# Performance work log

Measured on AMD Instinct MI355X. Metric: run time of the kernel, lower is better.

Reference implementation:

```python
import jax, jax.numpy as jnp
import numpy as np

WS, SS, P, H = 7, 3, 14, 12  # window, shift, patch grid, heads
NW = (P // WS) ** 2          # windows per image = 4
N_WIN = WS * WS              # tokens per window = 49

def _rel_pos_index():
    coords = np.stack(np.meshgrid(np.arange(WS), np.arange(WS), indexing='ij')).reshape(2, -1)
    rel = (coords[:, :, None] - coords[:, None, :]).transpose(1, 2, 0).astype(np.int64)
    rel[..., 0] += WS - 1
    rel[..., 1] += WS - 1
    rel[..., 0] *= 2 * WS - 1
    return rel.sum(-1)  # [49,49]

def _shift_mask():
    img = np.zeros((P, P))
    sl = (slice(0, -WS), slice(-WS, -SS), slice(-SS, None))
    cnt = 0
    for h in sl:
        for w in sl:
            img[h, w] = cnt
            cnt += 1
    mw = img.reshape(P // WS, WS, P // WS, WS).transpose(0, 2, 1, 3).reshape(-1, N_WIN)
    am = mw[:, None, :] - mw[:, :, None]
    return np.where(am != 0, -100.0, 0.0).astype(np.float32)  # [nW,49,49]

RPI = jnp.asarray(_rel_pos_index())
MASK = jnp.asarray(_shift_mask())

def _hswish(x):
    return x * jnp.clip(x + 3.0, 0.0, 6.0) / 6.0

def _hsig(x):
    return jnp.clip(x + 3.0, 0.0, 6.0) / 6.0

def _bn(x, g, b, eps=1e-5):
    # training-mode batchnorm over (B,H,W) per channel, biased variance
    m = x.mean((0, 2, 3), keepdims=True)
    v = ((x - m) ** 2).mean((0, 2, 3), keepdims=True)
    return (x - m) / jnp.sqrt(v + eps) * g[None, :, None, None] + b[None, :, None, None]

def setup_inputs() -> dict:
    key = jax.random.key(0)
    ks = jax.random.split(key, 20)
    C, HID = 768, 3072
    return {
        'x': jax.random.normal(ks[0], (32, 197, C), jnp.float32),
        'w_qkv': jax.random.normal(ks[1], (3 * C, C), jnp.float32) * 0.02,
        'w_proj': jax.random.normal(ks[2], (C, C), jnp.float32) * 0.02,
        'b_proj': jax.random.normal(ks[3], (C,), jnp.float32) * 0.02,
        'rpb_table': jax.random.normal(ks[4], ((2 * WS - 1) ** 2, H), jnp.float32) * 0.02,
        'pw1_w': jax.random.normal(ks[5], (HID, C), jnp.float32) * 0.02,
        'bn1_g': 1.0 + jax.random.normal(ks[6], (HID,), jnp.float32) * 0.02,
        'bn1_b': jax.random.normal(ks[7], (HID,), jnp.float32) * 0.02,
        'dw_w': jax.random.normal(ks[8], (HID, 3, 3), jnp.float32) * 0.1,
        'bn2_g': 1.0 + jax.random.normal(ks[9], (HID,), jnp.float32) * 0.02,
        'bn2_b': jax.random.normal(ks[10], (HID,), jnp.float32) * 0.02,
        'se_w1': jax.random.normal(ks[11], (HID // 4, HID), jnp.float32) * 0.02,
        'se_b1': jax.random.normal(ks[12], (HID // 4,), jnp.float32) * 0.02,
        'se_w2': jax.random.normal(ks[13], (HID, HID // 4), jnp.float32) * 0.02,
        'se_b2': jax.random.normal(ks[14], (HID,), jnp.float32) * 0.02,
        'pw2_w': jax.random.normal(ks[15], (C, HID), jnp.float32) * 0.02,
        'bn3_g': 1.0 + jax.random.normal(ks[16], (C,), jnp.float32) * 0.02,
        'bn3_b': jax.random.normal(ks[17], (C,), jnp.float32) * 0.02,
    }

def reference(x, w_qkv, w_proj, b_proj, rpb_table, pw1_w, bn1_g, bn1_b, dw_w,
              bn2_g, bn2_b, se_w1, se_b1, se_w2, se_b2, pw2_w, bn3_g, bn3_b):
    B, N, C = x.shape
    hd = C // H
    scale = hd ** -0.5
    nw = P // WS

    cls_tok = x[:, :1]
    xs = x[:, 1:].reshape(B, P, P, C)
    xs = jnp.roll(xs, (-SS, -SS), axis=(1, 2))  # cyclic shift
    # window partition -> [B*nW, 49, C]
    win = xs.reshape(B, nw, WS, nw, WS, C).transpose(0, 1, 3, 2, 4, 5).reshape(B * NW, N_WIN, C)

    qkv = (win @ w_qkv.T).reshape(B * NW, N_WIN, 3, H, hd).transpose(2, 0, 3, 1, 4)
    q, k, v = qkv[0], qkv[1], qkv[2]  # [B*nW, H, 49, hd]
    attn = jnp.einsum('bhqd,bhkd->bhqk', q, k) * scale
    # relative position bias gather: [H,49,49]
    bias = rpb_table[RPI.reshape(-1)].reshape(N_WIN, N_WIN, H).transpose(2, 0, 1)
    attn = attn + bias[None]
    # shifted-window mask add
    attn = (attn.reshape(B, NW, H, N_WIN, N_WIN) + MASK[None, :, None]).reshape(B * NW, H, N_WIN, N_WIN)
    attn = jax.nn.softmax(attn, axis=-1)
    out = jnp.einsum('bhqk,bhkd->bhqd', attn, v).transpose(0, 2, 1, 3).reshape(B * NW, N_WIN, C)
    out = out @ w_proj.T + b_proj

    # window reverse + reverse shift
    xs = out.reshape(B, nw, nw, WS, WS, C).transpose(0, 1, 3, 2, 4, 5).reshape(B, P, P, C)
    xs = jnp.roll(xs, (SS, SS), axis=(1, 2))
    x = jnp.concatenate([cls_tok, xs.reshape(B, P * P, C)], axis=1)

    # LocalityFeedForward (inverted residual conv MLP with SE)
    cls_tok, xt = x[:, :1], x[:, 1:]
    f = xt.transpose(0, 2, 1).reshape(B, C, P, P)
    h = _hswish(_bn(jnp.einsum('bchw,oc->bohw', f, pw1_w), bn1_g, bn1_b))
    h = _hswish(_bn(jax.lax.conv_general_dilated(
        h, dw_w[:, None], (1, 1), 'SAME',
        feature_group_count=h.shape[1],
        dimension_numbers=('NCHW', 'OIHW', 'NCHW')), bn2_g, bn2_b))
    s = h.mean((2, 3))  # global avg pool [B, hid]
    s = _hsig(jax.nn.relu(s @ se_w1.T + se_b1) @ se_w2.T + se_b2)
    h = h * s[:, :, None, None]
    h = _bn(jnp.einsum('bchw,oc->bohw', h, pw2_w), bn3_g, bn3_b)
    f = f + h
    x = jnp.concatenate([cls_tok, f.reshape(B, C, P * P).transpose(0, 2, 1)], axis=1)
    return x
```

## Files before the change

kernel.cpp:

```cpp
#include <hip/hip_runtime.h>
#include <hip/hip_bf16.h>

typedef unsigned short ushort_t;
typedef unsigned int uint_t;
typedef short short8 __attribute__((ext_vector_type(8)));
typedef float floatx4 __attribute__((ext_vector_type(4)));

__device__ inline float b2f(ushort_t u){
    uint_t v = ((uint_t)u) << 16;
    return __uint_as_float(v);
}
__device__ inline ushort_t f2b(float f){
    uint_t v = __float_as_uint(f);
    uint_t r = (v + 0x7FFFu + ((v >> 16) & 1u)) >> 16;
    return (ushort_t)r;
}
__device__ inline void unpack8(uint4 u, float* f){
    uint_t w[4] = {u.x, u.y, u.z, u.w};
    #pragma unroll
    for (int i = 0; i < 4; ++i){
        f[2*i]   = __uint_as_float(w[i] << 16);
        f[2*i+1] = __uint_as_float(w[i] & 0xFFFF0000u);
    }
}
__device__ inline uint4 pack8(const float* f){
    uint4 o;
    uint_t w[4];
    #pragma unroll
    for (int i = 0; i < 4; ++i)
        w[i] = (uint_t)f2b(f[2*i]) | ((uint_t)f2b(f[2*i+1]) << 16);
    o.x = w[0]; o.y = w[1]; o.z = w[2]; o.w = w[3];
    return o;
}
__device__ inline ushort4 cvt4(float4 v){
    ushort4 o;
    o.x = f2b(v.x); o.y = f2b(v.y); o.z = f2b(v.z); o.w = f2b(v.w);
    return o;
}
__device__ inline float hswish(float y){
    return y * fminf(fmaxf(y + 3.f, 0.f), 6.f) * (1.f/6.f);
}

#define MROWS 6272
#define CDIM  768
#define HID   3072
#define QKV3  2304

__device__ inline int scatter_row(int ri){
    int w  = ri / 49, t = ri % 49;
    int b  = w >> 2,  wi = w & 3;
    int wy = wi >> 1, wx = wi & 1;
    int ty = t / 7,   tx = t % 7;
    int yd = (wy*7 + ty + 3) % 14;
    int xd = (wx*7 + tx + 3) % 14;
    return b*196 + yd*14 + xd;
}

__global__ __launch_bounds__(256) void cvt_f2b(const float4* __restrict__ in,
                                               ushort4* __restrict__ out, int n4){
    int i = blockIdx.x * 256 + threadIdx.x;
    if (i < n4) out[i] = cvt4(in[i]);
}

__global__ __launch_bounds__(256) void dw_transpose(const float* __restrict__ w,
                                                    float* __restrict__ wT){
    int i = blockIdx.x*256 + threadIdx.x;
    if (i < HID*9){ int c = i/9, k = i%9; wT[k*HID + c] = w[i]; }
}

__global__ __launch_bounds__(256) void gather_win(const float4* __restrict__ x,
                                                  ushort4* __restrict__ win){
    int idx = blockIdx.x * 256 + threadIdx.x;
    if (idx >= MROWS * 192) return;
    int r  = idx / 192, c4 = idx % 192;
    int w  = r / 49,  t  = r % 49;
    int b  = w >> 2,  wi = w & 3;
    int wy = wi >> 1, wx = wi & 1;
    int ty = t / 7,   tx = t % 7;
    int ys = (wy*7 + ty + 3) % 14;
    int xs = (wx*7 + tx + 3) % 14;
    win[idx] = cvt4(x[(size_t)b*197*192 + (size_t)(1 + ys*14 + xs)*192 + c4]);
}

__global__ __launch_bounds__(256) void gemm_bt(const ushort_t* __restrict__ A,
                                               const ushort_t* __restrict__ B,
                                               ushort_t* __restrict__ Cb,
                                               float* __restrict__ Cf,
                                               int M, int N, int K,
                                               const float* __restrict__ bias,
                                               float* __restrict__ stats,
                                               int scat){
    const int nx   = gridDim.x;
    int flat = blockIdx.y * nx + blockIdx.x;
    int xcd  = flat & 7;
    int k    = flat >> 3;
    int by   = xcd + 8 * (k / nx);
    int bx   = k % nx;
    if (by * 128 >= M) return;

    __shared__ __align__(16) ushort_t As[2][128*32];
    __shared__ __align__(16) ushort_t Bs[2][128*32];
    const int tid  = threadIdx.x;
    const int lane = tid & 63;
    const int wid  = tid >> 6;
    const int m0 = by * 128;
    const int n0 = bx * 128;
    const int wm = (wid >> 1) * 64;
    const int wn = (wid & 1) * 64;

    const int srow = (lane >> 2);
    const int scol = (((lane & 3) ^ ((lane >> 3) & 3)) * 8);

    floatx4 acc[4][4] = {};

    auto stage = [&](int buf, int k0){
        #pragma unroll
        for (int j = 0; j < 2; ++j){
            int ch  = wid*2 + j;
            const ushort_t* gA = A + (size_t)(m0 + ch*16 + srow)*K + k0 + scol;
            const ushort_t* gB = B + (size_t)(n0 + ch*16 + srow)*K + k0 + scol;
            __builtin_amdgcn_global_load_lds(
                (const __attribute__((address_space(1))) void*)gA,
                (__attribute__((address_space(3))) void*)(&As[buf][ch*512 + lane*8]), 16, 0, 0);
            __builtin_amdgcn_global_load_lds(
                (const __attribute__((address_space(1))) void*)gB,
                (__attribute__((address_space(3))) void*)(&Bs[buf][ch*512 + lane*8]), 16, 0, 0);
        }
    };

    const int NK = K >> 5;
    stage(0, 0);

    const int fr   = lane & 15;
    const int quad = lane >> 4;
    const int cosw = (quad ^ ((fr >> 1) & 3)) * 8;
    int cur = 0;
    for (int it = 0; it < NK; ++it){
        __builtin_amdgcn_sched_barrier(0);
        __builtin_amdgcn_s_barrier();
        if (it + 1 < NK){
            stage(cur ^ 1, (it + 1) << 5);
            asm volatile("s_waitcnt vmcnt(4)" ::: "memory");
        } else {
            asm volatile("s_waitcnt vmcnt(0)" ::: "memory");
        }
        __builtin_amdgcn_s_barrier();
        __builtin_amdgcn_sched_barrier(0);

        short8 af[4], bfr[4];
        #pragma unroll
        for (int i = 0; i < 4; ++i){
            af[i]  = *(const short8*)(&As[cur][(wm + i*16 + fr)*32 + cosw]);
            bfr[i] = *(const short8*)(&Bs[cur][(wn + i*16 + fr)*32 + cosw]);
        }
        #pragma unroll
        for (int i = 0; i < 4; ++i)
            #pragma unroll
            for (int j = 0; j < 4; ++j)
                acc[i][j] = __builtin_amdgcn_mfma_f32_16x16x32_bf16(af[i], bfr[j], acc[i][j], 0, 0, 0);
        cur ^= 1;
    }

    if (!scat && Cb){
        __syncthreads();
        ushort_t* Cspace = (wid < 2) ? &As[0][0] : &Bs[0][0];
        #pragma unroll
        for (int i = 0; i < 4; ++i){
            #pragma unroll
            for (int j = 0; j < 4; ++j){
                int col = wn + j*16 + fr;
                float bv = bias ? bias[n0 + col] : 0.f;
                #pragma unroll
                for (int r = 0; r < 4; ++r)
                    Cspace[(i*16 + quad*4 + r)*128 + (col ^ (quad << 4))] =
                        f2b(acc[i][j][r] + bv);
            }
        }
        __syncthreads();
        #pragma unroll
        for (int q = 0; q < 8; ++q){
            int fl  = q*256 + tid;
            int row = fl >> 4, u4c = fl & 15;
            const ushort_t* srcRow = (row < 64) ? (&As[0][0] + row*128)
                                                : (&Bs[0][0] + (row - 64)*128);
            int g = (row >> 2) & 3;
            *(uint4*)(Cb + (size_t)(m0 + row)*N + n0 + u4c*8) =
                *(const uint4*)(srcRow + ((u4c*8) ^ (g << 4)));
        }
    } else {
        #pragma unroll
        for (int i = 0; i < 4; ++i){
            int grow = m0 + wm + i*16 + quad*4;
            #pragma unroll
            for (int j = 0; j < 4; ++j){
                int gcol = n0 + wn + j*16 + fr;
                float bv = bias ? bias[gcol] : 0.f;
                if (scat){
                    #pragma unroll
                    for (int r = 0; r < 4; ++r){
                        float v = acc[i][j][r] + bv;
                        size_t off = (size_t)scatter_row(grow + r)*N + gcol;
                        Cf[off] = v;
                        Cb[off] = f2b(v);
                    }
                } else {
                    #pragma unroll
                    for (int r = 0; r < 4; ++r)
                        Cf[(size_t)(grow + r)*N + gcol] = acc[i][j][r] + bv;
                }
            }
        }
    }

    if (stats){
        #pragma unroll
        for (int j = 0; j < 4; ++j){
            int gcol = n0 + wn + j*16 + fr;
            float bv = bias ? bias[gcol] : 0.f;
            float sv = 0.f, sq = 0.f;
            #pragma unroll
            for (int i = 0; i < 4; ++i)
                #pragma unroll
                for (int r = 0; r < 4; ++r){
                    float v = acc[i][j][r] + bv;
                    sv += v; sq += v*v;
                }
            sv += __shfl_xor(sv, 16, 64);  sq += __shfl_xor(sq, 16, 64);
            sv += __shfl_xor(sv, 32, 64);  sq += __shfl_xor(sq, 32, 64);
            if (lane < 16){
                atomicAdd(&stats[gcol], sv);
                atomicAdd(&stats[N + gcol], sq);
            }
        }
    }
}

__global__ __launch_bounds__(256) void gemm_bt64(const ushort_t* __restrict__ A,
                                                 const ushort_t* __restrict__ B,
                                                 ushort_t* __restrict__ Cb,
                                                 float* __restrict__ Cf,
                                                 int M, int N, int K,
                                                 const float* __restrict__ bias,
                                                 float* __restrict__ stats,
                                                 int scat){
    const int nx   = gridDim.x;
    int flat = blockIdx.y * nx + blockIdx.x;
    int xcd  = flat & 7;
    int k    = flat >> 3;
    int by   = xcd + 8 * (k / nx);
    int bx   = k % nx;
    if (by * 128 >= M) return;

    __shared__ __align__(16) ushort_t As[2][128*32];
    __shared__ __align__(16) ushort_t Bs[2][64*32];
    const int tid  = threadIdx.x;
    const int lane = tid & 63;
    const int wid  = tid >> 6;
    const int m0 = by * 128;
    const int n0 = bx * 64;
    const int wm = (wid >> 1) * 64;
    const int wn = (wid & 1) * 32;

    const int srow = (lane >> 2);
    const int scol = (((lane & 3) ^ ((lane >> 3) & 3)) * 8);

    floatx4 acc[4][2] = {};

    auto stage = [&](int buf, int k0){
        #pragma unroll
        for (int j = 0; j < 2; ++j){
            int ch = wid*2 + j;
            const ushort_t* gA = A + (size_t)(m0 + ch*16 + srow)*K + k0 + scol;
            __builtin_amdgcn_global_load_lds(
                (const __attribute__((address_space(1))) void*)gA,
                (__attribute__((address_space(3))) void*)(&As[buf][ch*512 + lane*8]), 16, 0, 0);
        }
        const ushort_t* gB = B + (size_t)(n0 + wid*16 + srow)*K + k0 + scol;
        __builtin_amdgcn_global_load_lds(
            (const __attribute__((address_space(1))) void*)gB,
            (__attribute__((address_space(3))) void*)(&Bs[buf][wid*512 + lane*8]), 16, 0, 0);
    };

    const int NK = K >> 5;
    stage(0, 0);

    const int fr   = lane & 15;
    const int quad = lane >> 4;
    const int cosw = (quad ^ ((fr >> 1) & 3)) * 8;
    int cur = 0;
    for (int it = 0; it < NK; ++it){
        __builtin_amdgcn_sched_barrier(0);
        __builtin_amdgcn_s_barrier();
        if (it + 1 < NK){
            stage(cur ^ 1, (it + 1) << 5);
            asm volatile("s_waitcnt vmcnt(3)" ::: "memory");
        } else {
            asm volatile("s_waitcnt vmcnt(0)" ::: "memory");
        }
        __builtin_amdgcn_s_barrier();
        __builtin_amdgcn_sched_barrier(0);

        short8 af[4], bfr[2];
        #pragma unroll
        for (int i = 0; i < 4; ++i)
            af[i]  = *(const short8*)(&As[cur][(wm + i*16 + fr)*32 + cosw]);
        #pragma unroll
        for (int j = 0; j < 2; ++j)
            bfr[j] = *(const short8*)(&Bs[cur][(wn + j*16 + fr)*32 + cosw]);
        #pragma unroll
        for (int i = 0; i < 4; ++i)
            #pragma unroll
            for (int j = 0; j < 2; ++j)
                acc[i][j] = __builtin_amdgcn_mfma_f32_16x16x32_bf16(af[i], bfr[j], acc[i][j], 0, 0, 0);
        cur ^= 1;
    }

    #pragma unroll
    for (int i = 0; i < 4; ++i){
        int grow = m0 + wm + i*16 + quad*4;
        #pragma unroll
        for (int j = 0; j < 2; ++j){
            int gcol = n0 + wn + j*16 + fr;
            float bv = bias ? bias[gcol] : 0.f;
            if (scat){
                #pragma unroll
                for (int r = 0; r < 4; ++r){
                    float v = acc[i][j][r] + bv;
                    size_t off = (size_t)scatter_row(grow + r)*N + gcol;
                    Cf[off] = v;
                    Cb[off] = f2b(v);
                }
            } else if (Cb){
                #pragma unroll
                for (int r = 0; r < 4; ++r)
                    Cb[(size_t)(grow + r)*N + gcol] = f2b(acc[i][j][r] + bv);
            } else {
                #pragma unroll
                for (int r = 0; r < 4; ++r)
                    Cf[(size_t)(grow + r)*N + gcol] = acc[i][j][r] + bv;
            }
        }
    }

    if (stats){
        #pragma unroll
        for (int j = 0; j < 2; ++j){
            int gcol = n0 + wn + j*16 + fr;
            float bv = bias ? bias[gcol] : 0.f;
            float sv = 0.f, sq = 0.f;
            #pragma unroll
            for (int i = 0; i < 4; ++i)
                #pragma unroll
                for (int r = 0; r < 4; ++r){
                    float v = acc[i][j][r] + bv;
                    sv += v; sq += v*v;
                }
            sv += __shfl_xor(sv, 16, 64);  sq += __shfl_xor(sq, 16, 64);
            sv += __shfl_xor(sv, 32, 64);  sq += __shfl_xor(sq, 32, 64);
            if (lane < 16){
                atomicAdd(&stats[gcol], sv);
                atomicAdd(&stats[N + gcol], sq);
            }
        }
    }
}

__global__ __launch_bounds__(256) void bm_precompute(const float* __restrict__ rpb,
                                                     float* __restrict__ bm){
    int idx = blockIdx.x*256 + threadIdx.x;
    if (idx >= 12*4*64*64) return;
    int ki = idx & 63, qi = (idx >> 6) & 63, wi = (idx >> 12) & 3, h = idx >> 14;
    float v = -1e30f;
    if (qi < 49 && ki < 49){
        int qy = qi/7, qx = qi%7, ky = ki/7, kx = ki%7;
        int ridx = (qy - ky + 6)*13 + (qx - kx + 6);
        v = rpb[ridx*12 + h];
        int wy = wi >> 1, wx = wi & 1;
        int gqy = wy*7 + qy, gqx = wx*7 + qx, gky = wy*7 + ky, gkx = wx*7 + kx;
        int cq = ((gqy < 7) ? 0 : (gqy < 11 ? 1 : 2))*3 + ((gqx < 7) ? 0 : (gqx < 11 ? 1 : 2));
        int ck = ((gky < 7) ? 0 : (gky < 11 ? 1 : 2))*3 + ((gkx < 7) ? 0 : (gkx < 11 ? 1 : 2));
        if (cq != ck) v -= 100.f;
    }
    bm[idx] = v;
}

__global__ __launch_bounds__(256) void attn_mfma(const ushort_t* __restrict__ qkv,
                                                 ushort_t* __restrict__ outp,
                                                 const float* __restrict__ bm){
    __shared__ __align__(16) ushort_t Ps[64*72];
    __shared__ __align__(16) ushort_t VT[64*72];
    const int tid = threadIdx.x, lane = tid & 63, wid = tid >> 6;
    const int h = blockIdx.x, w = blockIdx.y, wi = w & 3;
    const int fr = lane & 15, quad = lane >> 4, co = quad*8;

    for (int idx = tid; idx < 64*8; idx += 256){
        int k = idx >> 3, ng = idx & 7;
        uint4 u = {0u, 0u, 0u, 0u};
        if (k < 49) u = *(const uint4*)(qkv + (size_t)(w*49 + k)*QKV3 + 1536 + h*64 + ng*8);
        const ushort_t* vp = (const ushort_t*)&u;
        #pragma unroll
        for (int e = 0; e < 8; ++e) VT[(ng*8 + e)*72 + k] = vp[e];
    }
    __syncthreads();

    floatx4 accs[4] = {};
    const ushort_t* qbase = qkv + (size_t)(w*49 + wid*16 + fr)*QKV3 + h*64;
    #pragma unroll
    for (int k0 = 0; k0 < 64; k0 += 32){
        short8 af = *(const short8*)(qbase + k0 + co);
        #pragma unroll
        for (int j = 0; j < 4; ++j){
            const ushort_t* kbase = qkv + (size_t)(w*49 + j*16 + fr)*QKV3 + 768 + h*64;
            short8 bf = *(const short8*)(kbase + k0 + co);
            accs[j] = __builtin_amdgcn_mfma_f32_16x16x32_bf16(af, bf, accs[j], 0, 0, 0);
        }
    }

    const float* bmh = bm + (size_t)((h*4 + wi)*64 + wid*16)*64;
    #pragma unroll
    for (int r = 0; r < 4; ++r){
        int lrow = quad*4 + r;
        float m = -3e38f;
        #pragma unroll
        for (int j = 0; j < 4; ++j){
            float a = accs[j][r]*0.125f + bmh[lrow*64 + j*16 + fr];
            accs[j][r] = a;
            m = fmaxf(m, a);
        }
        #pragma unroll
        for (int off = 1; off < 16; off <<= 1) m = fmaxf(m, __shfl_xor(m, off, 64));
        float s = 0.f;
        #pragma unroll
        for (int j = 0; j < 4; ++j){
            float e = __expf(accs[j][r] - m);
            accs[j][r] = e; s += e;
        }
        #pragma unroll
        for (int off = 1; off < 16; off <<= 1) s += __shfl_xor(s, off, 64);
        float inv = 1.f / s;
        #pragma unroll
        for (int j = 0; j < 4; ++j)
            Ps[(wid*16 + lrow)*72 + j*16 + fr] = f2b(accs[j][r]*inv);
    }
    __syncthreads();

    floatx4 acco[4] = {};
    #pragma unroll
    for (int k0 = 0; k0 < 64; k0 += 32){
        short8 af = *(const short8*)(Ps + (wid*16 + fr)*72 + k0 + co);
        #pragma unroll
        for (int j = 0; j < 4; ++j){
            short8 bf = *(const short8*)(VT + (j*16 + fr)*72 + k0 + co);
            acco[j] = __builtin_amdgcn_mfma_f32_16x16x32_bf16(af, bf, acco[j], 0, 0, 0);
        }
    }
    #pragma unroll
    for (int r = 0; r < 4; ++r){
        int qi = wid*16 + quad*4 + r;
        if (qi < 49){
            #pragma unroll
            for (int j = 0; j < 4; ++j)
                outp[(size_t)(w*49 + qi)*CDIM + h*64 + j*16 + fr] = f2b(acco[j][r]);
        }
    }
}

__global__ void zero_f32(float* __restrict__ p, int n){
    int i = blockIdx.x*256 + threadIdx.x;
    if (i < n) p[i] = 0.f;
}
__global__ __launch_bounds__(256) void bn_stats_v(const ushort_t* __restrict__ X,
                                                  float* __restrict__ sums){
    const int cgl = threadIdx.x & 31;
    const int rp  = threadIdx.x >> 5;
    const int cg  = blockIdx.x*32 + cgl;
    const int r0  = blockIdx.y*224;
    const uint4* Xb = (const uint4*)X;
    float s[8] = {}, q[8] = {};
    for (int r = r0 + rp; r < r0 + 224; r += 8){
        uint4 u = Xb[(size_t)r*384 + cg];
        float f[8]; unpack8(u, f);
        #pragma unroll
        for (int e = 0; e < 8; ++e){ s[e] += f[e]; q[e] += f[e]*f[e]; }
    }
    #pragma unroll
    for (int e = 0; e < 8; ++e){
        s[e] += __shfl_xor(s[e], 32, 64);
        q[e] += __shfl_xor(q[e], 32, 64);
    }
    __shared__ float red[4][32][17];
    const int wv = threadIdx.x >> 6;
    if ((threadIdx.x & 32) == 0){
        #pragma unroll
        for (int e = 0; e < 8; ++e){
            red[wv][cgl][e]   = s[e];
            red[wv][cgl][8+e] = q[e];
        }
    }
    __syncthreads();
    #pragma unroll
    for (int k = 0; k < 2; ++k){
        int o = threadIdx.x*2 + k;
        int cgo = o >> 4, e = o & 15;
        float v = red[0][cgo][e] + red[1][cgo][e] + red[2][cgo][e] + red[3][cgo][e];
        int c = blockIdx.x*256 + cgo*8 + (e & 7);
        atomicAdd(&sums[(e < 8 ? 0 : HID) + c], v);
    }
}
__global__ void bn_finalize(float* __restrict__ sums, const float* __restrict__ g,
                            const float* __restrict__ b, int Cch){
    int c = blockIdx.x*256 + threadIdx.x;
    if (c >= Cch) return;
    float mean = sums[c] * (1.f/6272.f);
    float var  = sums[Cch + c] * (1.f/6272.f) - mean*mean;
    float sc = g[c] * rsqrtf(var + 1e-5f);
    sums[c] = sc;
    sums[Cch + c] = b[c] - mean*sc;
}

__global__ __launch_bounds__(256) void dwconv_v(const ushort_t* __restrict__ in,
                                                const float* __restrict__ wT,
                                                const float* __restrict__ ss,
                                                ushort_t* __restrict__ out){
    int idx = blockIdx.x*256 + threadIdx.x;
    if (idx >= MROWS*384) return;
    int r  = idx / 384, cg = idx % 384;
    int b  = r / 196,  p  = r % 196;
    int y  = p / 14,   x  = p % 14;
    int c  = cg*8;
    const uint4* inb = (const uint4*)(in + (size_t)b*196*HID);
    float sc[8], sh[8];
    {
        const float4* s0 = (const float4*)(ss + c);
        const float4* s1 = (const float4*)(ss + HID + c);
        float4 a0 = s0[0], a1 = s0[1], b0 = s1[0], b1 = s1[1];
        sc[0]=a0.x; sc[1]=a0.y; sc[2]=a0.z; sc[3]=a0.w;
        sc[4]=a1.x; sc[5]=a1.y; sc[6]=a1.z; sc[7]=a1.w;
        sh[0]=b0.x; sh[1]=b0.y; sh[2]=b0.z; sh[3]=b0.w;
        sh[4]=b1.x; sh[5]=b1.y; sh[6]=b1.z; sh[7]=b1.w;
    }
    float acc[8] = {};
    #pragma unroll
    for (int ky = 0; ky < 3; ++ky){
        int yy = y + ky - 1;
        if ((unsigned)yy >= 14u) continue;
        #pragma unroll
        for (int kx = 0; kx < 3; ++kx){
            int xx = x + kx - 1;
            if ((unsigned)xx >= 14u) continue;
            uint4 u = inb[(yy*14 + xx)*384 + cg];
            float fin[8]; unpack8(u, fin);
            const float4* wp = (const float4*)(wT + (ky*3 + kx)*HID + c);
            float4 w0 = wp[0], w1 = wp[1];
            float wv[8] = {w0.x,w0.y,w0.z,w0.w,w1.x,w1.y,w1.z,w1.w};
            #pragma unroll
            for (int e = 0; e < 8; ++e)
                acc[e] += hswish(fin[e]*sc[e] + sh[e]) * wv[e];
        }
    }
    ((uint4*)out)[idx] = pack8(acc);
}

__global__ __launch_bounds__(256) void se_mean_v(const ushort_t* __restrict__ X,
                                                 const float* __restrict__ ss,
                                                 float* __restrict__ s){
    const int b   = blockIdx.x;
    const int cgl = threadIdx.x & 31;
    const int rp  = threadIdx.x >> 5;
    const int cg  = blockIdx.y*32 + cgl;
    const int c   = cg*8;
    float sc[8], sh[8];
    #pragma unroll
    for (int e = 0; e < 8; ++e){ sc[e] = ss[c+e]; sh[e] = ss[HID+c+e]; }
    const uint4* Xb = (const uint4*)(X + (size_t)b*196*HID);
    float a[8] = {};
    for (int p = rp; p < 196; p += 8){
        uint4 u = Xb[(size_t)p*384 + cg];
        float f[8]; unpack8(u, f);
        #pragma unroll
        for (int e = 0; e < 8; ++e) a[e] += hswish(f[e]*sc[e] + sh[e]);
    }
    #pragma unroll
    for (int e = 0; e < 8; ++e) a[e] += __shfl_xor(a[e], 32, 64);
    __shared__ float red[4][32][9];
    const int wv = threadIdx.x >> 6;
    if ((threadIdx.x & 32) == 0){
        #pragma unroll
        for (int e = 0; e < 8; ++e) red[wv][cgl][e] = a[e];
    }
    __syncthreads();
    {
        int o = threadIdx.x;
        int cgo = o >> 3, e = o & 7;
        float v = red[0][cgo][e] + red[1][cgo][e] + red[2][cgo][e] + red[3][cgo][e];
        s[(size_t)b*HID + blockIdx.y*256 + cgo*8 + e] = v * (1.f/196.f);
    }
}
__global__ __launch_bounds__(256) void se_fc(const float* __restrict__ in,
                                             const float* __restrict__ w,
                                             const float* __restrict__ bias,
                                             float* __restrict__ out,
                                             int IN, int OUT, int mode){
    int wv   = (blockIdx.x*256 + threadIdx.x) >> 6;
    int lane = threadIdx.x & 63;
    if (wv >= OUT) return;
    const float* wr = w + (size_t)wv * IN;
    float acc[32];
    #pragma unroll
    for (int b = 0; b < 32; ++b) acc[b] = 0.f;
    for (int k = lane; k < IN; k += 64){
        float wval = wr[k];
        #pragma unroll
        for (int b = 0; b < 32; ++b)
            acc[b] += in[b*IN + k] * wval;
    }
    #pragma unroll
    for (int b = 0; b < 32; ++b){
        float v = acc[b];
        #pragma unroll
        for (int off = 32; off; off >>= 1) v += __shfl_down(v, off, 64);
        if (lane == 0){
            float a = v + bias[wv];
            if (mode == 0) a = fmaxf(a, 0.f);
            else           a = fminf(fmaxf(a + 3.f, 0.f), 6.f) * (1.f/6.f);
            out[b*OUT + wv] = a;
        }
    }
}
__global__ __launch_bounds__(256) void se_scale(ushort_t* __restrict__ X,
                                                const float* __restrict__ ss,
                                                const float* __restrict__ s2){
    int idx = blockIdx.x*256 + threadIdx.x;
    if (idx >= MROWS * (HID/8)) return;
    int r = idx / (HID/8), c8 = idx % (HID/8);
    int b = r / 196;
    int c = c8*8;
    uint4 u = ((uint4*)X)[idx];
    float f[8]; unpack8(u, f);
    const float* sp = s2 + b*HID + c;
    #pragma unroll
    for (int e = 0; e < 8; ++e)
        f[e] = hswish(f[e]*ss[c+e] + ss[HID+c+e]) * sp[e];
    ((uint4*)X)[idx] = pack8(f);
}

__global__ __launch_bounds__(256) void final_k(const float4* __restrict__ xin,
                                               const float4* __restrict__ f,
                                               const float4* __restrict__ h4,
                                               const float* __restrict__ ss,
                                               float4* __restrict__ outp){
    int idx = blockIdx.x*256 + threadIdx.x;
    if (idx >= 32*197*192) return;
    int b = idx / (197*192);
    int rem = idx % (197*192);
    int n = rem / 192, c4 = rem % 192;
    if (n == 0){ outp[idx] = xin[idx]; return; }
    size_t off = ((size_t)b*196 + n - 1)*192 + c4;
    float4 hv = h4[off];
    float4 fv = f[off];
    float4 o;
    int c = c4*4;
    o.x = fv.x + hv.x*ss[c+0] + ss[CDIM + c+0];
    o.y = fv.y + hv.y*ss[c+1] + ss[CDIM + c+1];
    o.z = fv.z + hv.z*ss[c+2] + ss[CDIM + c+2];
    o.w = fv.w + hv.w*ss[c+3] + ss[CDIM + c+3];
    outp[idx] = o;
}

extern "C" void kernel_launch(void* const* d_in, const int* in_sizes, int n_in,
                              void* d_out, int out_size, void* d_ws, size_t ws_size,
                              hipStream_t stream){
    const float* x      = (const float*)d_in[0];
    const float* w_qkv  = (const float*)d_in[1];
    const float* w_proj = (const float*)d_in[2];
    const float* b_proj = (const float*)d_in[3];
    const float* rpb    = (const float*)d_in[4];
    const float* pw1_w  = (const float*)d_in[5];
    const float* bn1_g  = (const float*)d_in[6];
    const float* bn1_b  = (const float*)d_in[7];
    const float* dw_w   = (const float*)d_in[8];
    const float* bn2_g  = (const float*)d_in[9];
    const float* bn2_b  = (const float*)d_in[10];
    const float* se_w1  = (const float*)d_in[11];
    const float* se_b1  = (const float*)d_in[12];
    const float* se_w2  = (const float*)d_in[13];
    const float* se_b2  = (const float*)d_in[14];
    const float* pw2_w  = (const float*)d_in[15];
    const float* bn3_g  = (const float*)d_in[16];
    const float* bn3_b  = (const float*)d_in[17];

    char* ws = (char*)d_ws;
    ushort_t* win    = (ushort_t*)(ws + 0);
    float*    bm     = (float*)(ws + 0);
    ushort_t* qkv    = (ushort_t*)(ws + 9633792);
    ushort_t* fbf    = (ushort_t*)(ws + 0);
    ushort_t* pw1b   = (ushort_t*)(ws + 9633792);
    ushort_t* hb     = (ushort_t*)(ws + 0);
    ushort_t* wqkvb  = (ushort_t*)(ws + 38535168);
    ushort_t* attnb  = (ushort_t*)(ws + 38535168);
    ushort_t* wprojb = (ushort_t*)(ws + 48168960);
    ushort_t* ha     = (ushort_t*)(ws + 38535168);
    float*    h4     = (float*)(ws + 38535168);
    ushort_t* pw2b   = (ushort_t*)(ws + 57802752);
    float*    f      = (float*)(ws + 77070336);
    float*    stats  = (float*)(ws + 96337920);
    float*    s      = (float*)(ws + 96362496);
    float*    s1     = (float*)(ws + 96755712);
    float*    s2     = (float*)(ws + 96854016);
    float*    dwwT   = (float*)(ws + 96854016);

    const int vec_rows = (MROWS*192 + 255)/256;
    const int vec_hid8 = (MROWS*(HID/8) + 255)/256;
    const int GY = 56;

    dw_transpose<<<(HID*9 + 255)/256, 256, 0, stream>>>(dw_w, dwwT);
    cvt_f2b<<<(QKV3*CDIM/4 + 255)/256, 256, 0, stream>>>((const float4*)w_qkv, (ushort4*)wqkvb, QKV3*CDIM/4);
    cvt_f2b<<<(CDIM*CDIM/4 + 255)/256, 256, 0, stream>>>((const float4*)w_proj, (ushort4*)wprojb, CDIM*CDIM/4);

    gather_win<<<vec_rows, 256, 0, stream>>>((const float4*)x, (ushort4*)win);
    gemm_bt<<<dim3(QKV3/128, GY), 256, 0, stream>>>(win, wqkvb, qkv, nullptr, MROWS, QKV3, CDIM, nullptr, nullptr, 0);
    bm_precompute<<<(12*4*64*64)/256, 256, 0, stream>>>(rpb, bm);
    attn_mfma<<<dim3(12, 128), 256, 0, stream>>>(qkv, attnb, bm);
    cvt_f2b<<<(HID*CDIM/4 + 255)/256, 256, 0, stream>>>((const float4*)pw1_w, (ushort4*)pw1b, HID*CDIM/4);
    zero_f32<<<24, 256, 0, stream>>>(stats, 2*HID);
    gemm_bt64<<<dim3(CDIM/64, GY), 256, 0, stream>>>(attnb, wprojb, fbf, f, MROWS, CDIM, CDIM, b_proj, nullptr, 1);

    gemm_bt<<<dim3(HID/128, GY), 256, 0, stream>>>(fbf, pw1b, ha, nullptr, MROWS, HID, CDIM, nullptr, stats, 0);
    bn_finalize<<<HID/256, 256, 0, stream>>>(stats, bn1_g, bn1_b, HID);

    dwconv_v<<<(MROWS*384 + 255)/256, 256, 0, stream>>>(ha, dwwT, stats, hb);
    cvt_f2b<<<(CDIM*HID/4 + 255)/256, 256, 0, stream>>>((const float4*)pw2_w, (ushort4*)pw2b, CDIM*HID/4);
    zero_f32<<<24, 256, 0, stream>>>(stats, 2*HID);
    bn_stats_v<<<dim3(12, 28), 256, 0, stream>>>(hb, stats);
    bn_finalize<<<HID/256, 256, 0, stream>>>(stats, bn2_g, bn2_b, HID);

    se_mean_v<<<dim3(32, 12), 256, 0, stream>>>(hb, stats, s);
    se_fc<<<dim3((CDIM*64)/256), 256, 0, stream>>>(s, se_w1, se_b1, s1, HID, CDIM, 0);
    se_fc<<<dim3((HID*64)/256), 256, 0, stream>>>(s1, se_w2, se_b2, s2, CDIM, HID, 1);
    se_scale<<<vec_hid8, 256, 0, stream>>>(hb, stats, s2);

    zero_f32<<<6, 256, 0, stream>>>(stats, 2*CDIM);
    gemm_bt64<<<dim3(CDIM/64, GY), 256, 0, stream>>>(hb, pw2b, nullptr, h4, MROWS, CDIM, HID, nullptr, stats, 0);
    bn_finalize<<<CDIM/256, 256, 0, stream>>>(stats, bn3_g, bn3_b, CDIM);
    final_k<<<(32*197*192 + 255)/256, 256, 0, stream>>>((const float4*)x, (const float4*)f, (const float4*)h4, stats, (float4*)d_out);
}
```

Baseline: 532.7 us.

## Fuse BN2 stats into dwconv, keep residual and pw2 output in bf16

The depthwise conv kernel now also accumulates per-channel sum and sum-of-squares and atomically adds them, which removes the separate bn_stats pass over the hidden activation. The proj GEMM writes only a bf16 residual instead of fp32 plus bf16. The pw2 GEMM writes bf16 through an LDS-staged, swizzled vectorized store in place of scattered fp32 stores, and the final kernel reads bf16 inputs 8 elements at a time. Stat buffers are zeroed once at the start. This cuts global memory traffic and launch count, at the cost of bf16 rounding of the residual and pw2 output and a dwconv grid with fewer, longer-running blocks.

```diff
diff --git a/kernel.cpp b/kernel.cpp
--- a/kernel.cpp
+++ b/kernel.cpp
@@ -200,7 +200,7 @@
                     for (int r = 0; r < 4; ++r){
                         float v = acc[i][j][r] + bv;
                         size_t off = (size_t)scatter_row(grow + r)*N + gcol;
-                        Cf[off] = v;
+                        if (Cf) Cf[off] = v;
                         Cb[off] = f2b(v);
                     }
                 } else {
@@ -315,29 +315,51 @@
         cur ^= 1;
     }
 
-    #pragma unroll
-    for (int i = 0; i < 4; ++i){
-        int grow = m0 + wm + i*16 + quad*4;
-        #pragma unroll
-        for (int j = 0; j < 2; ++j){
-            int gcol = n0 + wn + j*16 + fr;
-            float bv = bias ? bias[gcol] : 0.f;
-            if (scat){
-                #pragma unroll
-                for (int r = 0; r < 4; ++r){
-                    float v = acc[i][j][r] + bv;
-                    size_t off = (size_t)scatter_row(grow + r)*N + gcol;
-                    Cf[off] = v;
-                    Cb[off] = f2b(v);
-                }
-            } else if (Cb){
+    if (!scat && Cb){
+        __syncthreads();
+        ushort_t* Cst = &As[0][0];
+        #pragma unroll
+        for (int i = 0; i < 4; ++i){
+            #pragma unroll
+            for (int j = 0; j < 2; ++j){
+                int col = wn + j*16 + fr;
+                float bv = bias ? bias[n0 + col] : 0.f;
                 #pragma unroll
                 for (int r = 0; r < 4; ++r)
-                    Cb[(size_t)(grow + r)*N + gcol] = f2b(acc[i][j][r] + bv);
-            } else {
-                #pragma unroll
-                for (int r = 0; r < 4; ++r)
-                    Cf[(size_t)(grow + r)*N + gcol] = acc[i][j][r] + bv;
+                    Cst[(wm + i*16 + quad*4 + r)*64 + (col ^ (quad << 4))] =
+                        f2b(acc[i][j][r] + bv);
+            }
+        }
+        __syncthreads();
+        #pragma unroll
+        for (int q = 0; q < 4; ++q){
+            int fl  = q*256 + tid;
+            int row = fl >> 3, u4c = fl & 7;
+            int g = (row >> 2) & 3;
+            *(uint4*)(Cb + (size_t)(m0 + row)*N + n0 + u4c*8) =
+                *(const uint4*)(Cst + row*64 + ((u4c*8) ^ (g << 4)));
+        }
+    } else {
+        #pragma unroll
+        for (int i = 0; i < 4; ++i){
+            int grow = m0 + wm + i*16 + quad*4;
+            #pragma unroll
+            for (int j = 0; j < 2; ++j){
+                int gcol = n0 + wn + j*16 + fr;
+                float bv = bias ? bias[gcol] : 0.f;
+                if (scat){
+                    #pragma unroll
+                    for (int r = 0; r < 4; ++r){
+                        float v = acc[i][j][r] + bv;
+                        size_t off = (size_t)scatter_row(grow + r)*N + gcol;
+                        if (Cf) Cf[off] = v;
+                        Cb[off] = f2b(v);
+                    }
+                } else {
+                    #pragma unroll
+                    for (int r = 0; r < 4; ++r)
+                        Cf[(size_t)(grow + r)*N + gcol] = acc[i][j][r] + bv;
+                }
             }
         }
     }
@@ -469,44 +491,6 @@
     int i = blockIdx.x*256 + threadIdx.x;
     if (i < n) p[i] = 0.f;
 }
-__global__ __launch_bounds__(256) void bn_stats_v(const ushort_t* __restrict__ X,
-                                                  float* __restrict__ sums){
-    const int cgl = threadIdx.x & 31;
-    const int rp  = threadIdx.x >> 5;
-    const int cg  = blockIdx.x*32 + cgl;
-    const int r0  = blockIdx.y*224;
-    const uint4* Xb = (const uint4*)X;
-    float s[8] = {}, q[8] = {};
-    for (int r = r0 + rp; r < r0 + 224; r += 8){
-        uint4 u = Xb[(size_t)r*384 + cg];
-        float f[8]; unpack8(u, f);
-        #pragma unroll
-        for (int e = 0; e < 8; ++e){ s[e] += f[e]; q[e] += f[e]*f[e]; }
-    }
-    #pragma unroll
-    for (int e = 0; e < 8; ++e){
-        s[e] += __shfl_xor(s[e], 32, 64);
-        q[e] += __shfl_xor(q[e], 32, 64);
-    }
-    __shared__ float red[4][32][17];
-    const int wv = threadIdx.x >> 6;
-    if ((threadIdx.x & 32) == 0){
-        #pragma unroll
-        for (int e = 0; e < 8; ++e){
-            red[wv][cgl][e]   = s[e];
-            red[wv][cgl][8+e] = q[e];
-        }
-    }
-    __syncthreads();
-    #pragma unroll
-    for (int k = 0; k < 2; ++k){
-        int o = threadIdx.x*2 + k;
-        int cgo = o >> 4, e = o & 15;
-        float v = red[0][cgo][e] + red[1][cgo][e] + red[2][cgo][e] + red[3][cgo][e];
-        int c = blockIdx.x*256 + cgo*8 + (e & 7);
-        atomicAdd(&sums[(e < 8 ? 0 : HID) + c], v);
-    }
-}
 __global__ void bn_finalize(float* __restrict__ sums, const float* __restrict__ g,
                             const float* __restrict__ b, int Cch){
     int c = blockIdx.x*256 + threadIdx.x;
@@ -518,47 +502,75 @@
     sums[Cch + c] = b[c] - mean*sc;
 }
 
-__global__ __launch_bounds__(256) void dwconv_v(const ushort_t* __restrict__ in,
+__global__ __launch_bounds__(256) void dwconv_s(const ushort_t* __restrict__ in,
                                                 const float* __restrict__ wT,
                                                 const float* __restrict__ ss,
-                                                ushort_t* __restrict__ out){
-    int idx = blockIdx.x*256 + threadIdx.x;
-    if (idx >= MROWS*384) return;
-    int r  = idx / 384, cg = idx % 384;
-    int b  = r / 196,  p  = r % 196;
-    int y  = p / 14,   x  = p % 14;
-    int c  = cg*8;
-    const uint4* inb = (const uint4*)(in + (size_t)b*196*HID);
+                                                ushort_t* __restrict__ out,
+                                                float* __restrict__ sums){
+    const int cgl = threadIdx.x & 31;
+    const int rp  = threadIdx.x >> 5;
+    const int cg  = blockIdx.x*32 + cgl;
+    const int c   = cg*8;
+    const int r0  = blockIdx.y*112;
     float sc[8], sh[8];
-    {
-        const float4* s0 = (const float4*)(ss + c);
-        const float4* s1 = (const float4*)(ss + HID + c);
-        float4 a0 = s0[0], a1 = s0[1], b0 = s1[0], b1 = s1[1];
-        sc[0]=a0.x; sc[1]=a0.y; sc[2]=a0.z; sc[3]=a0.w;
-        sc[4]=a1.x; sc[5]=a1.y; sc[6]=a1.z; sc[7]=a1.w;
-        sh[0]=b0.x; sh[1]=b0.y; sh[2]=b0.z; sh[3]=b0.w;
-        sh[4]=b1.x; sh[5]=b1.y; sh[6]=b1.z; sh[7]=b1.w;
-    }
-    float acc[8] = {};
-    #pragma unroll
-    for (int ky = 0; ky < 3; ++ky){
-        int yy = y + ky - 1;
-        if ((unsigned)yy >= 14u) continue;
-        #pragma unroll
-        for (int kx = 0; kx < 3; ++kx){
-            int xx = x + kx - 1;
-            if ((unsigned)xx >= 14u) continue;
-            uint4 u = inb[(yy*14 + xx)*384 + cg];
-            float fin[8]; unpack8(u, fin);
-            const float4* wp = (const float4*)(wT + (ky*3 + kx)*HID + c);
-            float4 w0 = wp[0], w1 = wp[1];
-            float wv[8] = {w0.x,w0.y,w0.z,w0.w,w1.x,w1.y,w1.z,w1.w};
-            #pragma unroll
-            for (int e = 0; e < 8; ++e)
-                acc[e] += hswish(fin[e]*sc[e] + sh[e]) * wv[e];
-        }
-    }
-    ((uint4*)out)[idx] = pack8(acc);
+    #pragma unroll
+    for (int e = 0; e < 8; ++e){ sc[e] = ss[c+e]; sh[e] = ss[HID+c+e]; }
+    float wv[9][8];
+    #pragma unroll
+    for (int kk = 0; kk < 9; ++kk){
+        const float4* wp = (const float4*)(wT + kk*HID + c);
+        float4 w0 = wp[0], w1 = wp[1];
+        wv[kk][0]=w0.x; wv[kk][1]=w0.y; wv[kk][2]=w0.z; wv[kk][3]=w0.w;
+        wv[kk][4]=w1.x; wv[kk][5]=w1.y; wv[kk][6]=w1.z; wv[kk][7]=w1.w;
+    }
+    float s[8] = {}, q[8] = {};
+    for (int r = r0 + rp; r < r0 + 112; r += 8){
+        int b = r / 196, p = r % 196;
+        int y = p / 14,  x = p % 14;
+        const uint4* inb = (const uint4*)(in + (size_t)b*196*HID);
+        float acc[8] = {};
+        #pragma unroll
+        for (int ky = 0; ky < 3; ++ky){
+            int yy = y + ky - 1;
+            if ((unsigned)yy >= 14u) continue;
+            #pragma unroll
+            for (int kx = 0; kx < 3; ++kx){
+                int xx = x + kx - 1;
+                if ((unsigned)xx >= 14u) continue;
+                uint4 u = inb[(yy*14 + xx)*384 + cg];
+                float fin[8]; unpack8(u, fin);
+                #pragma unroll
+                for (int e = 0; e < 8; ++e)
+                    acc[e] += hswish(fin[e]*sc[e] + sh[e]) * wv[ky*3 + kx][e];
+            }
+        }
+        ((uint4*)out)[(size_t)r*384 + cg] = pack8(acc);
+        #pragma unroll
+        for (int e = 0; e < 8; ++e){ s[e] += acc[e]; q[e] += acc[e]*acc[e]; }
+    }
+    #pragma unroll
+    for (int e = 0; e < 8; ++e){
+        s[e] += __shfl_xor(s[e], 32, 64);
+        q[e] += __shfl_xor(q[e], 32, 64);
+    }
+    __shared__ float red[4][32][17];
+    const int wvv = threadIdx.x >> 6;
+    if ((threadIdx.x & 32) == 0){
+        #pragma unroll
+        for (int e = 0; e < 8; ++e){
+            red[wvv][cgl][e]   = s[e];
+            red[wvv][cgl][8+e] = q[e];
+        }
+    }
+    __syncthreads();
+    #pragma unroll
+    for (int k = 0; k < 2; ++k){
+        int o = threadIdx.x*2 + k;
+        int cgo = o >> 4, e = o & 15;
+        float v = red[0][cgo][e] + red[1][cgo][e] + red[2][cgo][e] + red[3][cgo][e];
+        int cc = blockIdx.x*256 + cgo*8 + (e & 7);
+        atomicAdd(&sums[(e < 8 ? 0 : HID) + cc], v);
+    }
 }
 
 __global__ __launch_bounds__(256) void se_mean_v(const ushort_t* __restrict__ X,
@@ -645,26 +657,38 @@
 }
 
 __global__ __launch_bounds__(256) void final_k(const float4* __restrict__ xin,
-                                               const float4* __restrict__ f,
-                                               const float4* __restrict__ h4,
+                                               const ushort_t* __restrict__ fb,
+                                               const ushort_t* __restrict__ hb4,
                                                const float* __restrict__ ss,
                                                float4* __restrict__ outp){
     int idx = blockIdx.x*256 + threadIdx.x;
-    if (idx >= 32*197*192) return;
-    int b = idx / (197*192);
-    int rem = idx % (197*192);
-    int n = rem / 192, c4 = rem % 192;
-    if (n == 0){ outp[idx] = xin[idx]; return; }
-    size_t off = ((size_t)b*196 + n - 1)*192 + c4;
-    float4 hv = h4[off];
-    float4 fv = f[off];
-    float4 o;
-    int c = c4*4;
-    o.x = fv.x + hv.x*ss[c+0] + ss[CDIM + c+0];
-    o.y = fv.y + hv.y*ss[c+1] + ss[CDIM + c+1];
-    o.z = fv.z + hv.z*ss[c+2] + ss[CDIM + c+2];
-    o.w = fv.w + hv.w*ss[c+3] + ss[CDIM + c+3];
-    outp[idx] = o;
+    if (idx >= 32*197*96) return;
+    int b = idx / (197*96);
+    int rem = idx % (197*96);
+    int n = rem / 96, c8 = rem % 96;
+    size_t obase = ((size_t)b*197 + n)*192 + c8*2;
+    if (n == 0){
+        outp[obase]     = xin[obase];
+        outp[obase + 1] = xin[obase + 1];
+        return;
+    }
+    size_t off = ((size_t)b*196 + n - 1)*96 + c8;
+    uint4 fu = ((const uint4*)fb)[off];
+    uint4 hu = ((const uint4*)hb4)[off];
+    float fv[8], hv[8];
+    unpack8(fu, fv); unpack8(hu, hv);
+    int c = c8*8;
+    float4 o0, o1;
+    o0.x = fv[0] + hv[0]*ss[c+0] + ss[CDIM + c+0];
+    o0.y = fv[1] + hv[1]*ss[c+1] + ss[CDIM + c+1];
+    o0.z = fv[2] + hv[2]*ss[c+2] + ss[CDIM + c+2];
+    o0.w = fv[3] + hv[3]*ss[c+3] + ss[CDIM + c+3];
+    o1.x = fv[4] + hv[4]*ss[c+4] + ss[CDIM + c+4];
+    o1.y = fv[5] + hv[5]*ss[c+5] + ss[CDIM + c+5];
+    o1.z = fv[6] + hv[6]*ss[c+6] + ss[CDIM + c+6];
+    o1.w = fv[7] + hv[7]*ss[c+7] + ss[CDIM + c+7];
+    outp[obase]     = o0;
+    outp[obase + 1] = o1;
 }
 
 extern "C" void kernel_launch(void* const* d_in, const int* in_sizes, int n_in,
@@ -692,17 +716,18 @@
     char* ws = (char*)d_ws;
     ushort_t* win    = (ushort_t*)(ws + 0);
     float*    bm     = (float*)(ws + 0);
+    ushort_t* hb     = (ushort_t*)(ws + 0);
     ushort_t* qkv    = (ushort_t*)(ws + 9633792);
-    ushort_t* fbf    = (ushort_t*)(ws + 0);
     ushort_t* pw1b   = (ushort_t*)(ws + 9633792);
-    ushort_t* hb     = (ushort_t*)(ws + 0);
     ushort_t* wqkvb  = (ushort_t*)(ws + 38535168);
     ushort_t* attnb  = (ushort_t*)(ws + 38535168);
+    ushort_t* ha     = (ushort_t*)(ws + 38535168);
+    ushort_t* hb4    = (ushort_t*)(ws + 38535168);
     ushort_t* wprojb = (ushort_t*)(ws + 48168960);
-    ushort_t* ha     = (ushort_t*)(ws + 38535168);
-    float*    h4     = (float*)(ws + 38535168);
     ushort_t* pw2b   = (ushort_t*)(ws + 57802752);
-    float*    f      = (float*)(ws + 77070336);
+    ushort_t* fb2    = (ushort_t*)(ws + 77070336);
+    float*    stats2 = (float*)(ws + 86704128);
+    float*    stats3 = (float*)(ws + 86728704);
     float*    stats  = (float*)(ws + 96337920);
     float*    s      = (float*)(ws + 96362496);
     float*    s1     = (float*)(ws + 96755712);
@@ -713,6 +738,8 @@
     const int vec_hid8 = (MROWS*(HID/8) + 255)/256;
     const int GY = 56;
 
+    zero_f32<<<24, 256, 0, stream>>>(stats, 2*HID);
+    zero_f32<<<27, 256, 0, stream>>>(stats2, 2*HID + 2*CDIM);
     dw_transpose<<<(HID*9 + 255)/256, 256, 0, stream>>>(dw_w, dwwT);
     cvt_f2b<<<(QKV3*CDIM/4 + 255)/256, 256, 0, stream>>>((const float4*)w_qkv, (ushort4*)wqkvb, QKV3*CDIM/4);
     cvt_f2b<<<(CDIM*CDIM/4 + 255)/256, 256, 0, stream>>>((const float4*)w_proj, (ushort4*)wprojb, CDIM*CDIM/4);
@@ -722,25 +749,21 @@
     bm_precompute<<<(12*4*64*64)/256, 256, 0, stream>>>(rpb, bm);
     attn_mfma<<<dim3(12, 128), 256, 0, stream>>>(qkv, attnb, bm);
     cvt_f2b<<<(HID*CDIM/4 + 255)/256, 256, 0, stream>>>((const float4*)pw1_w, (ushort4*)pw1b, HID*CDIM/4);
-    zero_f32<<<24, 256, 0, stream>>>(stats, 2*HID);
-    gemm_bt64<<<dim3(CDIM/64, GY), 256, 0, stream>>>(attnb, wprojb, fbf, f, MROWS, CDIM, CDIM, b_proj, nullptr, 1);
-
-    gemm_bt<<<dim3(HID/128, GY), 256, 0, stream>>>(fbf, pw1b, ha, nullptr, MROWS, HID, CDIM, nullptr, stats, 0);
+    gemm_bt64<<<dim3(CDIM/64, GY), 256, 0, stream>>>(attnb, wprojb, fb2, nullptr, MROWS, CDIM, CDIM, b_proj, nullptr, 1);
+
+    gemm_bt<<<dim3(HID/128, GY), 256, 0, stream>>>(fb2, pw1b, ha, nullptr, MROWS, HID, CDIM, nullptr, stats, 0);
     bn_finalize<<<HID/256, 256, 0, stream>>>(stats, bn1_g, bn1_b, HID);
 
-    dwconv_v<<<(MROWS*384 + 255)/256, 256, 0, stream>>>(ha, dwwT, stats, hb);
+    dwconv_s<<<dim3(12, GY), 256, 0, stream>>>(ha, dwwT, stats, hb, stats2);
     cvt_f2b<<<(CDIM*HID/4 + 255)/256, 256, 0, stream>>>((const float4*)pw2_w, (ushort4*)pw2b, CDIM*HID/4);
-    zero_f32<<<24, 256, 0, stream>>>(stats, 2*HID);
-    bn_stats_v<<<dim3(12, 28), 256, 0, stream>>>(hb, stats);
-    bn_finalize<<<HID/256, 256, 0, stream>>>(stats, bn2_g, bn2_b, HID);
-
-    se_mean_v<<<dim3(32, 12), 256, 0, stream>>>(hb, stats, s);
+    bn_finalize<<<HID/256, 256, 0, stream>>>(stats2, bn2_g, bn2_b, HID);
+
+    se_mean_v<<<dim3(32, 12), 256, 0, stream>>>(hb, stats2, s);
     se_fc<<<dim3((CDIM*64)/256), 256, 0, stream>>>(s, se_w1, se_b1, s1, HID, CDIM, 0);
     se_fc<<<dim3((HID*64)/256), 256, 0, stream>>>(s1, se_w2, se_b2, s2, CDIM, HID, 1);
-    se_scale<<<vec_hid8, 256, 0, stream>>>(hb, stats, s2);
-
-    zero_f32<<<6, 256, 0, stream>>>(stats, 2*CDIM);
-    gemm_bt64<<<dim3(CDIM/64, GY), 256, 0, stream>>>(hb, pw2b, nullptr, h4, MROWS, CDIM, HID, nullptr, stats, 0);
-    bn_finalize<<<CDIM/256, 256, 0, stream>>>(stats, bn3_g, bn3_b, CDIM);
-    final_k<<<(32*197*192 + 255)/256, 256, 0, stream>>>((const float4*)x, (const float4*)f, (const float4*)h4, stats, (float4*)d_out);
-}
+    se_scale<<<vec_hid8, 256, 0, stream>>>(hb, stats2, s2);
+
+    gemm_bt64<<<dim3(CDIM/64, GY), 256, 0, stream>>>(hb, pw2b, hb4, nullptr, MROWS, CDIM, HID, nullptr, stats3, 0);
+    bn_finalize<<<CDIM/256, 256, 0, stream>>>(stats3, bn3_g, bn3_b, CDIM);
+    final_k<<<(32*197*96 + 255)/256, 256, 0, stream>>>((const float4*)x, fb2, hb4, stats3, (float4*)d_out);
+}
```

Result: faster. 521.8 us (-2.0%).
